# Kernel optimization log

Hardware: AMD Instinct MI355X
Metric: run time of the kernel (lower is better)

The kernel has to match this reference:

```python
import jax, jax.numpy as jnp
import numpy as np

BS, IN_SIZE, OUT_SIZE, FEATS = 32, 1024, 1024, 2048


def setup_inputs() -> dict:
    key = jax.random.key(0)
    kx, kw = jax.random.split(key)
    x = jax.random.normal(kx, (BS, IN_SIZE, FEATS), dtype=jnp.float32)
    # Per-sample weight matrices (the stacked nn.Parameters, kernel-size-1 conv
    # weights of shape [out_size, in_size, 1] -> squeezed to [out_size, in_size]).
    weights = jax.random.normal(kw, (BS, OUT_SIZE, IN_SIZE), dtype=jnp.float32)
    return {"x": x, "weights": weights}


def reference(x, weights):
    # F.conv2d(x.view(1, bs*in_size, feats), W.view(bs*out_size, in_size, 1), groups=bs)
    # with kernel size 1 is exactly a per-sample matmul:
    # out[b, o, f] = sum_i weights[b, o, i] * x[b, i, f]
    return jnp.einsum('boi,bif->bof', weights, x)
```

## Files before the change

### kernel.cpp

```cpp
#include <hip/hip_runtime.h>
#include <hip/hip_bf16.h>
#include <string.h>


typedef float  f32x2 __attribute__((ext_vector_type(2)));
typedef float  f32x4 __attribute__((ext_vector_type(4)));
typedef short  bf16x8 __attribute__((ext_vector_type(8)));
typedef unsigned int u32;

#define BATCH 32
#define MDIM 1024
#define KDIM 1024
#define NDIM 2048
#define BM 256
#define BN 256
#define BK 64
#define NT (KDIM / BK)
#define LSTR 68

__device__ __forceinline__ u32 cvt2(float a, float b) {
    float2 t; t.x = a; t.y = b;
    __hip_bfloat162 h = __float22bfloat162_rn(t);
    u32 r; memcpy(&r, &h, 4);
    return r;
}

__device__ __forceinline__ void lds_barrier() {
    asm volatile("s_waitcnt lgkmcnt(0)" ::: "memory");
    __builtin_amdgcn_s_barrier();
    asm volatile("" ::: "memory");
}

__global__ __launch_bounds__(512, 2) void bgemm_bf16_kernel(
    const float* __restrict__ x, const float* __restrict__ w,
    float* __restrict__ out)
{
    __shared__ unsigned short Ab[2][BM * LSTR];
    __shared__ unsigned short Bb[2][BN * LSTR];

    const int bid  = blockIdx.x;
    const int lbid = (bid & 7) * 128 + (bid >> 3);
    const int bx = lbid & 7;
    const int by = (lbid >> 3) & 3;
    const int bz = lbid >> 5;

    const int tid = threadIdx.x;
    const int m0  = by * BM;
    const int n0  = bx * BN;

    const int lane = tid & 63;
    const int wid  = tid >> 6;
    const int wm   = (wid >> 2) * 128;
    const int wn   = (wid & 3)  * 64;
    const int l15  = lane & 15;
    const int kg8  = (lane >> 4) * 8;

    const float* Ag = w + (size_t)bz * MDIM * KDIM + (size_t)m0 * KDIM;
    const float* Bg = x + (size_t)bz * KDIM * NDIM + n0;
    float*       Cg = out + (size_t)bz * MDIM * NDIM + (size_t)m0 * NDIM + n0;

    const int a_k4 = tid & 15;
    const int a_m0 = tid >> 4;
    int a_idx[8];
    #pragma unroll
    for (int i = 0; i < 8; ++i)
        a_idx[i] = (a_m0 + 32 * i) * LSTR + 4 * a_k4;
    const int bn0  = 2 * (tid & 127);
    const int b_k0 = 8 * (tid >> 7);
    int b_idx[2];
    #pragma unroll
    for (int c = 0; c < 2; ++c)
        b_idx[c] = (bn0 + c) * LSTR + b_k0;
    int rd_a[8], rd_b[4];
    #pragma unroll
    for (int mi = 0; mi < 8; ++mi)
        rd_a[mi] = (wm + mi * 16 + l15) * LSTR + kg8;
    #pragma unroll
    for (int ni = 0; ni < 4; ++ni)
        rd_b[ni] = (wn + ni * 16 + l15) * LSTR + kg8;

    const float* Ap = Ag + (size_t)a_m0 * KDIM + 4 * a_k4;
    const float* Bp = Bg + (size_t)b_k0 * NDIM + bn0;

    f32x4 acc[8][4];
    #pragma unroll
    for (int i = 0; i < 8; ++i)
        #pragma unroll
        for (int j = 0; j < 4; ++j)
            acc[i][j] = f32x4{0.f, 0.f, 0.f, 0.f};

    f32x4 aav[4];
    f32x2 bbv[8];

    auto load_regs = [&](int kt, int h) {
        #pragma unroll
        for (int i = 0; i < 4; ++i)
            aav[i] = *reinterpret_cast<const f32x4*>(
                Ap + (size_t)(32 * (i + 4 * h)) * KDIM + kt);
        #pragma unroll
        for (int j = 0; j < 8; ++j)
            bbv[j] = *reinterpret_cast<const f32x2*>(
                Bp + (size_t)(kt + 32 * h + j) * NDIM);
    };
    auto stage = [&](int s, int h) {
        #pragma unroll
        for (int i = 0; i < 4; ++i) {
            uint2 v = make_uint2(cvt2(aav[i][0], aav[i][1]),
                                 cvt2(aav[i][2], aav[i][3]));
            *reinterpret_cast<uint2*>(&Ab[s][a_idx[i + 4 * h]]) = v;
        }
        #pragma unroll
        for (int c = 0; c < 2; ++c) {
            uint4 v = make_uint4(cvt2(bbv[0][c], bbv[1][c]),
                                 cvt2(bbv[2][c], bbv[3][c]),
                                 cvt2(bbv[4][c], bbv[5][c]),
                                 cvt2(bbv[6][c], bbv[7][c]));
            *reinterpret_cast<uint4*>(&Bb[s][b_idx[c] + 32 * h]) = v;
        }
    };

    load_regs(0, 0);
    stage(0, 0);
    load_regs(0, 1);
    stage(0, 1);
    load_regs(BK, 0);
    lds_barrier();

    for (int t = 0; t < NT - 1; ++t) {
        const int cur = t & 1;
        const int ktn = (t + 1) * BK;
        bf16x8 bfr[4], af[4];

        #pragma unroll
        for (int ni = 0; ni < 4; ++ni)
            bfr[ni] = *reinterpret_cast<const bf16x8*>(&Bb[cur][rd_b[ni]]);
        #pragma unroll
        for (int mi = 0; mi < 4; ++mi)
            af[mi] = *reinterpret_cast<const bf16x8*>(&Ab[cur][rd_a[mi]]);

        stage(cur ^ 1, 0);
        load_regs(ktn, 1);

        __builtin_amdgcn_s_setprio(1);
        #pragma unroll
        for (int mi = 0; mi < 4; ++mi)
            #pragma unroll
            for (int ni = 0; ni < 4; ++ni)
                acc[mi][ni] = __builtin_amdgcn_mfma_f32_16x16x32_bf16(
                    af[mi], bfr[ni], acc[mi][ni], 0, 0, 0);
        __builtin_amdgcn_s_setprio(0);

        #pragma unroll
        for (int mi = 0; mi < 4; ++mi)
            af[mi] = *reinterpret_cast<const bf16x8*>(&Ab[cur][rd_a[mi + 4]]);

        __builtin_amdgcn_s_setprio(1);
        #pragma unroll
        for (int mi = 0; mi < 4; ++mi)
            #pragma unroll
            for (int ni = 0; ni < 4; ++ni)
                acc[mi + 4][ni] = __builtin_amdgcn_mfma_f32_16x16x32_bf16(
                    af[mi], bfr[ni], acc[mi + 4][ni], 0, 0, 0);
        __builtin_amdgcn_s_setprio(0);

        #pragma unroll
        for (int ni = 0; ni < 4; ++ni)
            bfr[ni] = *reinterpret_cast<const bf16x8*>(&Bb[cur][rd_b[ni] + 32]);
        #pragma unroll
        for (int mi = 0; mi < 4; ++mi)
            af[mi] = *reinterpret_cast<const bf16x8*>(&Ab[cur][rd_a[mi] + 32]);

        stage(cur ^ 1, 1);
        int kt2 = (t + 2) * BK;
        if (kt2 > KDIM - BK) kt2 = KDIM - BK;
        load_regs(kt2, 0);

        __builtin_amdgcn_s_setprio(1);
        #pragma unroll
        for (int mi = 0; mi < 4; ++mi)
            #pragma unroll
            for (int ni = 0; ni < 4; ++ni)
                acc[mi][ni] = __builtin_amdgcn_mfma_f32_16x16x32_bf16(
                    af[mi], bfr[ni], acc[mi][ni], 0, 0, 0);
        __builtin_amdgcn_s_setprio(0);

        #pragma unroll
        for (int mi = 0; mi < 4; ++mi)
            af[mi] = *reinterpret_cast<const bf16x8*>(&Ab[cur][rd_a[mi + 4] + 32]);

        __builtin_amdgcn_s_setprio(1);
        #pragma unroll
        for (int mi = 0; mi < 4; ++mi)
            #pragma unroll
            for (int ni = 0; ni < 4; ++ni)
                acc[mi + 4][ni] = __builtin_amdgcn_mfma_f32_16x16x32_bf16(
                    af[mi], bfr[ni], acc[mi + 4][ni], 0, 0, 0);
        __builtin_amdgcn_s_setprio(0);

        lds_barrier();
    }

    {
        const int cur = (NT - 1) & 1;
        #pragma unroll
        for (int kk = 0; kk < 2; ++kk) {
            bf16x8 bfr[4];
            #pragma unroll
            for (int ni = 0; ni < 4; ++ni)
                bfr[ni] = *reinterpret_cast<const bf16x8*>(
                    &Bb[cur][rd_b[ni] + 32 * kk]);
            #pragma unroll
            for (int mi = 0; mi < 8; ++mi) {
                bf16x8 af = *reinterpret_cast<const bf16x8*>(
                    &Ab[cur][rd_a[mi] + 32 * kk]);
                #pragma unroll
                for (int ni = 0; ni < 4; ++ni)
                    acc[mi][ni] = __builtin_amdgcn_mfma_f32_16x16x32_bf16(
                        af, bfr[ni], acc[mi][ni], 0, 0, 0);
            }
        }
    }

    const int rbase = (lane >> 4) * 4;
    #pragma unroll
    for (int mi = 0; mi < 8; ++mi) {
        #pragma unroll
        for (int ni = 0; ni < 4; ++ni) {
            int n  = wn + ni * 16 + l15;
            int mb = wm + mi * 16 + rbase;
            #pragma unroll
            for (int r = 0; r < 4; ++r)
                Cg[(size_t)(mb + r) * NDIM + n] = acc[mi][ni][r];
        }
    }
}

extern "C" void kernel_launch(void* const* d_in, const int* in_sizes, int n_in,
                              void* d_out, int out_size, void* d_ws, size_t ws_size,
                              hipStream_t stream) {
    const float* x = (const float*)d_in[0];
    const float* w = (const float*)d_in[1];
    float* out = (float*)d_out;
    const int nblocks = (NDIM / BN) * (MDIM / BM) * BATCH;
    bgemm_bf16_kernel<<<dim3(nblocks), dim3(512), 0, stream>>>(x, w, out);
}
```

Measured before the change: 231.9 us.

## Restructure main loop into barrier-separated load/stage/MFMA phases with split A/B loads

Splits the global-load and LDS-staging helpers into separate A and B versions and reorganizes each K iteration into four phases. Each phase issues LDS reads plus one global load or staging step, then an MFMA burst, with barriers around every burst. The goal is to keep waves in lock-step so memory and matrix work interleave across the waves of the workgroup, ping-pong style. In exchange it adds many more workgroup barriers per iteration and larger staging register arrays (8 A vectors, 16 B vectors), which may reduce occupancy or stall the MFMA pipe.

```diff
diff --git a/kernel.cpp b/kernel.cpp
--- a/kernel.cpp
+++ b/kernel.cpp
@@ -89,114 +89,106 @@
         for (int j = 0; j < 4; ++j)
             acc[i][j] = f32x4{0.f, 0.f, 0.f, 0.f};
 
-    f32x4 aav[4];
-    f32x2 bbv[8];
-
-    auto load_regs = [&](int kt, int h) {
-        #pragma unroll
-        for (int i = 0; i < 4; ++i)
+    f32x4 aav[8];
+    f32x2 bbv[16];
+
+    auto load_A = [&](int kt) {
+        #pragma unroll
+        for (int i = 0; i < 8; ++i)
             aav[i] = *reinterpret_cast<const f32x4*>(
-                Ap + (size_t)(32 * (i + 4 * h)) * KDIM + kt);
-        #pragma unroll
-        for (int j = 0; j < 8; ++j)
-            bbv[j] = *reinterpret_cast<const f32x2*>(
-                Bp + (size_t)(kt + 32 * h + j) * NDIM);
-    };
-    auto stage = [&](int s, int h) {
-        #pragma unroll
-        for (int i = 0; i < 4; ++i) {
+                Ap + (size_t)(32 * i) * KDIM + kt);
+    };
+    auto load_B = [&](int kt) {
+        #pragma unroll
+        for (int j = 0; j < 8; ++j) {
+            bbv[j]     = *reinterpret_cast<const f32x2*>(
+                Bp + (size_t)(kt + j) * NDIM);
+            bbv[j + 8] = *reinterpret_cast<const f32x2*>(
+                Bp + (size_t)(kt + 32 + j) * NDIM);
+        }
+    };
+    auto stage_A = [&](int s) {
+        #pragma unroll
+        for (int i = 0; i < 8; ++i) {
             uint2 v = make_uint2(cvt2(aav[i][0], aav[i][1]),
                                  cvt2(aav[i][2], aav[i][3]));
-            *reinterpret_cast<uint2*>(&Ab[s][a_idx[i + 4 * h]]) = v;
-        }
+            *reinterpret_cast<uint2*>(&Ab[s][a_idx[i]]) = v;
+        }
+    };
+    auto stage_B = [&](int s) {
         #pragma unroll
         for (int c = 0; c < 2; ++c) {
-            uint4 v = make_uint4(cvt2(bbv[0][c], bbv[1][c]),
-                                 cvt2(bbv[2][c], bbv[3][c]),
-                                 cvt2(bbv[4][c], bbv[5][c]),
-                                 cvt2(bbv[6][c], bbv[7][c]));
-            *reinterpret_cast<uint4*>(&Bb[s][b_idx[c] + 32 * h]) = v;
-        }
-    };
-
-    load_regs(0, 0);
-    stage(0, 0);
-    load_regs(0, 1);
-    stage(0, 1);
-    load_regs(BK, 0);
+            uint4 v0 = make_uint4(cvt2(bbv[0][c], bbv[1][c]),
+                                  cvt2(bbv[2][c], bbv[3][c]),
+                                  cvt2(bbv[4][c], bbv[5][c]),
+                                  cvt2(bbv[6][c], bbv[7][c]));
+            *reinterpret_cast<uint4*>(&Bb[s][b_idx[c]]) = v0;
+            uint4 v1 = make_uint4(cvt2(bbv[8][c],  bbv[9][c]),
+                                  cvt2(bbv[10][c], bbv[11][c]),
+                                  cvt2(bbv[12][c], bbv[13][c]),
+                                  cvt2(bbv[14][c], bbv[15][c]));
+            *reinterpret_cast<uint4*>(&Bb[s][b_idx[c] + 32]) = v1;
+        }
+    };
+    auto mfma4 = [&](int mb, const bf16x8* afr, const bf16x8* bfr) {
+        __builtin_amdgcn_s_setprio(1);
+        #pragma unroll
+        for (int mi = 0; mi < 4; ++mi)
+            #pragma unroll
+            for (int ni = 0; ni < 4; ++ni)
+                acc[mb + mi][ni] = __builtin_amdgcn_mfma_f32_16x16x32_bf16(
+                    afr[mi], bfr[ni], acc[mb + mi][ni], 0, 0, 0);
+        __builtin_amdgcn_s_setprio(0);
+    };
+
+    load_A(0);
+    load_B(0);
+    stage_A(0);
+    stage_B(0);
     lds_barrier();
 
     for (int t = 0; t < NT - 1; ++t) {
         const int cur = t & 1;
+        const int nxt = cur ^ 1;
         const int ktn = (t + 1) * BK;
-        bf16x8 bfr[4], af[4];
+        bf16x8 afr[4], bfr[4];
 
         #pragma unroll
         for (int ni = 0; ni < 4; ++ni)
             bfr[ni] = *reinterpret_cast<const bf16x8*>(&Bb[cur][rd_b[ni]]);
         #pragma unroll
         for (int mi = 0; mi < 4; ++mi)
-            af[mi] = *reinterpret_cast<const bf16x8*>(&Ab[cur][rd_a[mi]]);
-
-        stage(cur ^ 1, 0);
-        load_regs(ktn, 1);
-
-        __builtin_amdgcn_s_setprio(1);
-        #pragma unroll
-        for (int mi = 0; mi < 4; ++mi)
-            #pragma unroll
-            for (int ni = 0; ni < 4; ++ni)
-                acc[mi][ni] = __builtin_amdgcn_mfma_f32_16x16x32_bf16(
-                    af[mi], bfr[ni], acc[mi][ni], 0, 0, 0);
-        __builtin_amdgcn_s_setprio(0);
-
-        #pragma unroll
-        for (int mi = 0; mi < 4; ++mi)
-            af[mi] = *reinterpret_cast<const bf16x8*>(&Ab[cur][rd_a[mi + 4]]);
-
-        __builtin_amdgcn_s_setprio(1);
-        #pragma unroll
-        for (int mi = 0; mi < 4; ++mi)
-            #pragma unroll
-            for (int ni = 0; ni < 4; ++ni)
-                acc[mi + 4][ni] = __builtin_amdgcn_mfma_f32_16x16x32_bf16(
-                    af[mi], bfr[ni], acc[mi + 4][ni], 0, 0, 0);
-        __builtin_amdgcn_s_setprio(0);
+            afr[mi] = *reinterpret_cast<const bf16x8*>(&Ab[cur][rd_a[mi]]);
+        load_A(ktn);
+        lds_barrier();
+        mfma4(0, afr, bfr);
+        lds_barrier();
+
+        #pragma unroll
+        for (int mi = 0; mi < 4; ++mi)
+            afr[mi] = *reinterpret_cast<const bf16x8*>(&Ab[cur][rd_a[mi + 4]]);
+        stage_A(nxt);
+        load_B(ktn);
+        lds_barrier();
+        mfma4(4, afr, bfr);
+        lds_barrier();
 
         #pragma unroll
         for (int ni = 0; ni < 4; ++ni)
             bfr[ni] = *reinterpret_cast<const bf16x8*>(&Bb[cur][rd_b[ni] + 32]);
         #pragma unroll
         for (int mi = 0; mi < 4; ++mi)
-            af[mi] = *reinterpret_cast<const bf16x8*>(&Ab[cur][rd_a[mi] + 32]);
-
-        stage(cur ^ 1, 1);
-        int kt2 = (t + 2) * BK;
-        if (kt2 > KDIM - BK) kt2 = KDIM - BK;
-        load_regs(kt2, 0);
-
-        __builtin_amdgcn_s_setprio(1);
-        #pragma unroll
-        for (int mi = 0; mi < 4; ++mi)
-            #pragma unroll
-            for (int ni = 0; ni < 4; ++ni)
-                acc[mi][ni] = __builtin_amdgcn_mfma_f32_16x16x32_bf16(
-                    af[mi], bfr[ni], acc[mi][ni], 0, 0, 0);
-        __builtin_amdgcn_s_setprio(0);
-
-        #pragma unroll
-        for (int mi = 0; mi < 4; ++mi)
-            af[mi] = *reinterpret_cast<const bf16x8*>(&Ab[cur][rd_a[mi + 4] + 32]);
-
-        __builtin_amdgcn_s_setprio(1);
-        #pragma unroll
-        for (int mi = 0; mi < 4; ++mi)
-            #pragma unroll
-            for (int ni = 0; ni < 4; ++ni)
-                acc[mi + 4][ni] = __builtin_amdgcn_mfma_f32_16x16x32_bf16(
-                    af[mi], bfr[ni], acc[mi + 4][ni], 0, 0, 0);
-        __builtin_amdgcn_s_setprio(0);
-
+            afr[mi] = *reinterpret_cast<const bf16x8*>(&Ab[cur][rd_a[mi] + 32]);
+        stage_B(nxt);
+        lds_barrier();
+        mfma4(0, afr, bfr);
+        lds_barrier();
+
+        #pragma unroll
+        for (int mi = 0; mi < 4; ++mi)
+            afr[mi] = *reinterpret_cast<const bf16x8*>(&Ab[cur][rd_a[mi + 4] + 32]);
+        lds_barrier();
+        mfma4(4, afr, bfr);
         lds_barrier();
     }
 
```

New measurement: 323.1 us. +39.3%, slower.

## Pre-convert inputs to bf16 and stream tiles via direct global-to-LDS loads

Applied to the files above, without the earlier changes.

Adds two pre-pass kernels: one converts the weights to bf16, the other converts x to bf16 and transposes it to K-contiguous layout in the workspace. The GEMM then loads tiles with global_load_lds straight into swizzled LDS, which removes per-tile register staging and the in-loop conversion. The main loop is reorganised into four phases, each issuing a partial prefetch, with vmcnt waits and extra barriers between them. The cost is an extra fp32 read plus bf16 write of both inputs each call and more barriers. If the workspace is too small, an fp32 fallback kernel runs instead.

```diff
diff --git a/kernel.cpp b/kernel.cpp
--- a/kernel.cpp
+++ b/kernel.cpp
@@ -7,16 +7,12 @@
 typedef float  f32x4 __attribute__((ext_vector_type(4)));
 typedef short  bf16x8 __attribute__((ext_vector_type(8)));
 typedef unsigned int u32;
+typedef unsigned short u16;
 
 #define BATCH 32
 #define MDIM 1024
 #define KDIM 1024
 #define NDIM 2048
-#define BM 256
-#define BN 256
-#define BK 64
-#define NT (KDIM / BK)
-#define LSTR 68
 
 __device__ __forceinline__ u32 cvt2(float a, float b) {
     float2 t; t.x = a; t.y = b;
@@ -25,18 +21,68 @@
     return r;
 }
 
-__device__ __forceinline__ void lds_barrier() {
-    asm volatile("s_waitcnt lgkmcnt(0)" ::: "memory");
-    __builtin_amdgcn_s_barrier();
-    asm volatile("" ::: "memory");
-}
-
-__global__ __launch_bounds__(512, 2) void bgemm_bf16_kernel(
-    const float* __restrict__ x, const float* __restrict__ w,
+__global__ __launch_bounds__(256) void conv_w_kernel(
+    const float* __restrict__ w, u16* __restrict__ wb)
+{
+    const int nt = gridDim.x * blockDim.x;
+    const int total = BATCH * MDIM * KDIM / 4;
+    for (int i = blockIdx.x * blockDim.x + threadIdx.x; i < total; i += nt) {
+        f32x4 v = *reinterpret_cast<const f32x4*>(w + (size_t)i * 4);
+        uint2 p = make_uint2(cvt2(v[0], v[1]), cvt2(v[2], v[3]));
+        *reinterpret_cast<uint2*>(wb + (size_t)i * 4) = p;
+    }
+}
+
+__global__ __launch_bounds__(256) void conv_xt_kernel(
+    const float* __restrict__ x, u16* __restrict__ xb)
+{
+    __shared__ u16 tl[64][72];
+
+    const int bz = blockIdx.z;
+    const int k0 = blockIdx.y * 64;
+    const int n0 = blockIdx.x * 64;
+    const int t  = threadIdx.x;
+    const int a  = t >> 4;
+    const int b  = t & 15;
+
+    f32x4 v[4];
+    #pragma unroll
+    for (int i = 0; i < 4; ++i)
+        v[i] = *reinterpret_cast<const f32x4*>(
+            x + ((size_t)(bz * KDIM + k0 + 4 * a + i)) * NDIM + n0 + 4 * b);
+
+    #pragma unroll
+    for (int j = 0; j < 4; ++j) {
+        uint2 p = make_uint2(cvt2(v[0][j], v[1][j]), cvt2(v[2][j], v[3][j]));
+        *reinterpret_cast<uint2*>(&tl[4 * b + j][4 * a]) = p;
+    }
+    __syncthreads();
+
+    const int rn = t >> 2;
+    const int q  = t & 3;
+    u16* dst = xb + ((size_t)(bz * NDIM + n0 + rn)) * KDIM + k0 + 16 * q;
+    *reinterpret_cast<uint4*>(dst)     = *reinterpret_cast<uint4*>(&tl[rn][16 * q]);
+    *reinterpret_cast<uint4*>(dst + 8) = *reinterpret_cast<uint4*>(&tl[rn][16 * q + 8]);
+}
+
+#define BM 256
+#define BN 256
+#define BK 64
+#define NT2 (KDIM / BK)
+
+typedef __attribute__((address_space(1))) const unsigned char glob_u8;
+typedef __attribute__((address_space(3))) unsigned char lds_u8;
+
+__device__ __forceinline__ void gload16(const void* g, void* l) {
+    __builtin_amdgcn_global_load_lds((glob_u8*)g, (lds_u8*)l, 16, 0, 0);
+}
+
+__global__ __launch_bounds__(512, 2) void bgemm_4ph_kernel(
+    const u16* __restrict__ xb, const u16* __restrict__ wb,
     float* __restrict__ out)
 {
-    __shared__ unsigned short Ab[2][BM * LSTR];
-    __shared__ unsigned short Bb[2][BN * LSTR];
+    __shared__ u16 Al[2][16384];
+    __shared__ u16 Bl[2][16384];
 
     const int bid  = blockIdx.x;
     const int lbid = (bid & 7) * 128 + (bid >> 3);
@@ -44,43 +90,46 @@
     const int by = (lbid >> 3) & 3;
     const int bz = lbid >> 5;
 
-    const int tid = threadIdx.x;
-    const int m0  = by * BM;
-    const int n0  = bx * BN;
-
+    const int tid  = threadIdx.x;
+    const int wid  = tid >> 6;
     const int lane = tid & 63;
-    const int wid  = tid >> 6;
     const int wm   = (wid >> 2) * 128;
     const int wn   = (wid & 3)  * 64;
     const int l15  = lane & 15;
-    const int kg8  = (lane >> 4) * 8;
-
-    const float* Ag = w + (size_t)bz * MDIM * KDIM + (size_t)m0 * KDIM;
-    const float* Bg = x + (size_t)bz * KDIM * NDIM + n0;
-    float*       Cg = out + (size_t)bz * MDIM * NDIM + (size_t)m0 * NDIM + n0;
-
-    const int a_k4 = tid & 15;
-    const int a_m0 = tid >> 4;
-    int a_idx[8];
-    #pragma unroll
-    for (int i = 0; i < 8; ++i)
-        a_idx[i] = (a_m0 + 32 * i) * LSTR + 4 * a_k4;
-    const int bn0  = 2 * (tid & 127);
-    const int b_k0 = 8 * (tid >> 7);
-    int b_idx[2];
-    #pragma unroll
-    for (int c = 0; c < 2; ++c)
-        b_idx[c] = (bn0 + c) * LSTR + b_k0;
-    int rd_a[8], rd_b[4];
-    #pragma unroll
-    for (int mi = 0; mi < 8; ++mi)
-        rd_a[mi] = (wm + mi * 16 + l15) * LSTR + kg8;
-    #pragma unroll
-    for (int ni = 0; ni < 4; ++ni)
-        rd_b[ni] = (wn + ni * 16 + l15) * LSTR + kg8;
-
-    const float* Ap = Ag + (size_t)a_m0 * KDIM + 4 * a_k4;
-    const float* Bp = Bg + (size_t)b_k0 * NDIM + bn0;
+    const int h    = lane >> 4;
+
+    const int m0 = by * BM;
+    const int n0 = bx * BN;
+
+    const u16* Wb = wb + ((size_t)bz << 20);
+    const u16* Xb = xb + ((size_t)bz << 21);
+
+    const int srow = wid * 32 + (lane >> 2);
+    const int ssw  = 8 * ((lane & 3) ^ ((lane >> 2) & 3));
+    const u16* aSrc[2];
+    const u16* bSrc[2];
+    #pragma unroll
+    for (int i = 0; i < 2; ++i) {
+        aSrc[i] = Wb + (size_t)(m0 + srow + i * 16) * KDIM + ssw;
+        bSrc[i] = Xb + (size_t)(n0 + srow + i * 16) * KDIM + ssw;
+    }
+    const int ldst0 = wid * 1024 + 0 * 512;
+    const int ldst1 = wid * 1024 + 1 * 512;
+
+    int rdA[2][8], rdB[2][4];
+    #pragma unroll
+    for (int kk = 0; kk < 2; ++kk) {
+        #pragma unroll
+        for (int mi = 0; mi < 8; ++mi) {
+            int m = wm + mi * 16 + l15;
+            rdA[kk][mi] = kk * 8192 + m * 32 + 8 * (h ^ (m & 3));
+        }
+        #pragma unroll
+        for (int ni = 0; ni < 4; ++ni) {
+            int n = wn + ni * 16 + l15;
+            rdB[kk][ni] = kk * 8192 + n * 32 + 8 * (h ^ (n & 3));
+        }
+    }
 
     f32x4 acc[8][4];
     #pragma unroll
@@ -89,138 +138,102 @@
         for (int j = 0; j < 4; ++j)
             acc[i][j] = f32x4{0.f, 0.f, 0.f, 0.f};
 
-    f32x4 aav[4];
-    f32x2 bbv[8];
-
-    auto load_regs = [&](int kt, int h) {
-        #pragma unroll
-        for (int i = 0; i < 4; ++i)
-            aav[i] = *reinterpret_cast<const f32x4*>(
-                Ap + (size_t)(32 * (i + 4 * h)) * KDIM + kt);
-        #pragma unroll
-        for (int j = 0; j < 8; ++j)
-            bbv[j] = *reinterpret_cast<const f32x2*>(
-                Bp + (size_t)(kt + 32 * h + j) * NDIM);
-    };
-    auto stage = [&](int s, int h) {
-        #pragma unroll
-        for (int i = 0; i < 4; ++i) {
-            uint2 v = make_uint2(cvt2(aav[i][0], aav[i][1]),
-                                 cvt2(aav[i][2], aav[i][3]));
-            *reinterpret_cast<uint2*>(&Ab[s][a_idx[i + 4 * h]]) = v;
-        }
-        #pragma unroll
-        for (int c = 0; c < 2; ++c) {
-            uint4 v = make_uint4(cvt2(bbv[0][c], bbv[1][c]),
-                                 cvt2(bbv[2][c], bbv[3][c]),
-                                 cvt2(bbv[4][c], bbv[5][c]),
-                                 cvt2(bbv[6][c], bbv[7][c]));
-            *reinterpret_cast<uint4*>(&Bb[s][b_idx[c] + 32 * h]) = v;
-        }
-    };
-
-    load_regs(0, 0);
-    stage(0, 0);
-    load_regs(0, 1);
-    stage(0, 1);
-    load_regs(BK, 0);
-    lds_barrier();
-
-    for (int t = 0; t < NT - 1; ++t) {
-        const int cur = t & 1;
+    auto stageA = [&](int sb, int q, int kt) {
+        gload16(aSrc[0] + kt + q * 32, &Al[sb][q * 8192 + ldst0]);
+        gload16(aSrc[1] + kt + q * 32, &Al[sb][q * 8192 + ldst1]);
+    };
+    auto stageB = [&](int sb, int q, int kt) {
+        gload16(bSrc[0] + kt + q * 32, &Bl[sb][q * 8192 + ldst0]);
+        gload16(bSrc[1] + kt + q * 32, &Bl[sb][q * 8192 + ldst1]);
+    };
+
+    stageA(0, 0, 0);
+    stageB(0, 0, 0);
+    stageA(0, 1, 0);
+    stageB(0, 1, 0);
+    asm volatile("s_waitcnt vmcnt(4)" ::: "memory");
+    __builtin_amdgcn_s_barrier();
+
+    for (int t = 0; t < NT2; ++t) {
+        const int s   = t & 1;
+        const int sx  = s ^ 1;
         const int ktn = (t + 1) * BK;
-        bf16x8 bfr[4], af[4];
+        const bool st = (t + 1 < NT2);
+        bf16x8 afr[4], bfr[4];
 
         #pragma unroll
         for (int ni = 0; ni < 4; ++ni)
-            bfr[ni] = *reinterpret_cast<const bf16x8*>(&Bb[cur][rd_b[ni]]);
-        #pragma unroll
-        for (int mi = 0; mi < 4; ++mi)
-            af[mi] = *reinterpret_cast<const bf16x8*>(&Ab[cur][rd_a[mi]]);
-
-        stage(cur ^ 1, 0);
-        load_regs(ktn, 1);
-
+            bfr[ni] = *reinterpret_cast<const bf16x8*>(&Bl[s][rdB[0][ni]]);
+        #pragma unroll
+        for (int mi = 0; mi < 4; ++mi)
+            afr[mi] = *reinterpret_cast<const bf16x8*>(&Al[s][rdA[0][mi]]);
+        if (st) stageA(sx, 0, ktn);
+        __builtin_amdgcn_s_barrier();
         __builtin_amdgcn_s_setprio(1);
         #pragma unroll
         for (int mi = 0; mi < 4; ++mi)
             #pragma unroll
             for (int ni = 0; ni < 4; ++ni)
                 acc[mi][ni] = __builtin_amdgcn_mfma_f32_16x16x32_bf16(
-                    af[mi], bfr[ni], acc[mi][ni], 0, 0, 0);
+                    afr[mi], bfr[ni], acc[mi][ni], 0, 0, 0);
         __builtin_amdgcn_s_setprio(0);
-
-        #pragma unroll
-        for (int mi = 0; mi < 4; ++mi)
-            af[mi] = *reinterpret_cast<const bf16x8*>(&Ab[cur][rd_a[mi + 4]]);
-
+        __builtin_amdgcn_s_barrier();
+
+        #pragma unroll
+        for (int mi = 0; mi < 4; ++mi)
+            afr[mi] = *reinterpret_cast<const bf16x8*>(&Al[s][rdA[0][mi + 4]]);
+        if (st) stageB(sx, 0, ktn);
+        if (t == NT2 - 1)
+            asm volatile("s_waitcnt vmcnt(0)" ::: "memory");
+        else
+            asm volatile("s_waitcnt vmcnt(4)" ::: "memory");
+        __builtin_amdgcn_s_barrier();
         __builtin_amdgcn_s_setprio(1);
         #pragma unroll
         for (int mi = 0; mi < 4; ++mi)
             #pragma unroll
             for (int ni = 0; ni < 4; ++ni)
                 acc[mi + 4][ni] = __builtin_amdgcn_mfma_f32_16x16x32_bf16(
-                    af[mi], bfr[ni], acc[mi + 4][ni], 0, 0, 0);
+                    afr[mi], bfr[ni], acc[mi + 4][ni], 0, 0, 0);
         __builtin_amdgcn_s_setprio(0);
+        __builtin_amdgcn_s_barrier();
 
         #pragma unroll
         for (int ni = 0; ni < 4; ++ni)
-            bfr[ni] = *reinterpret_cast<const bf16x8*>(&Bb[cur][rd_b[ni] + 32]);
-        #pragma unroll
-        for (int mi = 0; mi < 4; ++mi)
-            af[mi] = *reinterpret_cast<const bf16x8*>(&Ab[cur][rd_a[mi] + 32]);
-
-        stage(cur ^ 1, 1);
-        int kt2 = (t + 2) * BK;
-        if (kt2 > KDIM - BK) kt2 = KDIM - BK;
-        load_regs(kt2, 0);
-
+            bfr[ni] = *reinterpret_cast<const bf16x8*>(&Bl[s][rdB[1][ni]]);
+        #pragma unroll
+        for (int mi = 0; mi < 4; ++mi)
+            afr[mi] = *reinterpret_cast<const bf16x8*>(&Al[s][rdA[1][mi]]);
+        if (st) stageA(sx, 1, ktn);
+        __builtin_amdgcn_s_barrier();
         __builtin_amdgcn_s_setprio(1);
         #pragma unroll
         for (int mi = 0; mi < 4; ++mi)
             #pragma unroll
             for (int ni = 0; ni < 4; ++ni)
                 acc[mi][ni] = __builtin_amdgcn_mfma_f32_16x16x32_bf16(
-                    af[mi], bfr[ni], acc[mi][ni], 0, 0, 0);
+                    afr[mi], bfr[ni], acc[mi][ni], 0, 0, 0);
         __builtin_amdgcn_s_setprio(0);
-
-        #pragma unroll
-        for (int mi = 0; mi < 4; ++mi)
-            af[mi] = *reinterpret_cast<const bf16x8*>(&Ab[cur][rd_a[mi + 4] + 32]);
-
+        __builtin_amdgcn_s_barrier();
+
+        #pragma unroll
+        for (int mi = 0; mi < 4; ++mi)
+            afr[mi] = *reinterpret_cast<const bf16x8*>(&Al[s][rdA[1][mi + 4]]);
+        if (st) stageB(sx, 1, ktn);
+        asm volatile("s_waitcnt vmcnt(4)" ::: "memory");
+        __builtin_amdgcn_s_barrier();
         __builtin_amdgcn_s_setprio(1);
         #pragma unroll
         for (int mi = 0; mi < 4; ++mi)
             #pragma unroll
             for (int ni = 0; ni < 4; ++ni)
                 acc[mi + 4][ni] = __builtin_amdgcn_mfma_f32_16x16x32_bf16(
-                    af[mi], bfr[ni], acc[mi + 4][ni], 0, 0, 0);
+                    afr[mi], bfr[ni], acc[mi + 4][ni], 0, 0, 0);
         __builtin_amdgcn_s_setprio(0);
-
-        lds_barrier();
-    }
-
-    {
-        const int cur = (NT - 1) & 1;
-        #pragma unroll
-        for (int kk = 0; kk < 2; ++kk) {
-            bf16x8 bfr[4];
-            #pragma unroll
-            for (int ni = 0; ni < 4; ++ni)
-                bfr[ni] = *reinterpret_cast<const bf16x8*>(
-                    &Bb[cur][rd_b[ni] + 32 * kk]);
-            #pragma unroll
-            for (int mi = 0; mi < 8; ++mi) {
-                bf16x8 af = *reinterpret_cast<const bf16x8*>(
-                    &Ab[cur][rd_a[mi] + 32 * kk]);
-                #pragma unroll
-                for (int ni = 0; ni < 4; ++ni)
-                    acc[mi][ni] = __builtin_amdgcn_mfma_f32_16x16x32_bf16(
-                        af, bfr[ni], acc[mi][ni], 0, 0, 0);
-            }
-        }
-    }
-
+        __builtin_amdgcn_s_barrier();
+    }
+
+    float* Cg = out + (size_t)bz * MDIM * NDIM + (size_t)(m0)*NDIM + n0;
     const int rbase = (lane >> 4) * 4;
     #pragma unroll
     for (int mi = 0; mi < 8; ++mi) {
@@ -233,6 +246,123 @@
                 Cg[(size_t)(mb + r) * NDIM + n] = acc[mi][ni][r];
         }
     }
+}
+
+#define FLSTR 68
+
+__device__ __forceinline__ void lds_barrier() {
+    asm volatile("s_waitcnt lgkmcnt(0)" ::: "memory");
+    __builtin_amdgcn_s_barrier();
+    asm volatile("" ::: "memory");
+}
+
+__global__ __launch_bounds__(512, 2) void bgemm_fb_kernel(
+    const float* __restrict__ x, const float* __restrict__ w,
+    float* __restrict__ out)
+{
+    __shared__ u16 Ab[2][BM * FLSTR];
+    __shared__ u16 Bb[2][BN * FLSTR];
+
+    const int bid  = blockIdx.x;
+    const int lbid = (bid & 7) * 128 + (bid >> 3);
+    const int bx = lbid & 7, by = (lbid >> 3) & 3, bz = lbid >> 5;
+    const int tid = threadIdx.x, lane = tid & 63, wid = tid >> 6;
+    const int wm = (wid >> 2) * 128, wn = (wid & 3) * 64;
+    const int l15 = lane & 15, kg8 = (lane >> 4) * 8;
+
+    const float* Ag = w + (size_t)bz * MDIM * KDIM + (size_t)(by * BM) * KDIM;
+    const float* Bg = x + (size_t)bz * KDIM * NDIM + bx * BN;
+    float* Cg = out + (size_t)bz * MDIM * NDIM + (size_t)(by * BM) * NDIM + bx * BN;
+
+    const int a_k4 = tid & 15, a_m0 = tid >> 4;
+    int a_idx[8];
+    #pragma unroll
+    for (int i = 0; i < 8; ++i) a_idx[i] = (a_m0 + 32 * i) * FLSTR + 4 * a_k4;
+    const int bn0 = 2 * (tid & 127), b_k0 = 8 * (tid >> 7);
+    int b_idx[2];
+    #pragma unroll
+    for (int c = 0; c < 2; ++c) b_idx[c] = (bn0 + c) * FLSTR + b_k0;
+    int rd_a[8], rd_b[4];
+    #pragma unroll
+    for (int mi = 0; mi < 8; ++mi) rd_a[mi] = (wm + mi * 16 + l15) * FLSTR + kg8;
+    #pragma unroll
+    for (int ni = 0; ni < 4; ++ni) rd_b[ni] = (wn + ni * 16 + l15) * FLSTR + kg8;
+
+    const float* Ap = Ag + (size_t)a_m0 * KDIM + 4 * a_k4;
+    const float* Bp = Bg + (size_t)b_k0 * NDIM + bn0;
+
+    f32x4 acc[8][4];
+    #pragma unroll
+    for (int i = 0; i < 8; ++i)
+        #pragma unroll
+        for (int j = 0; j < 4; ++j) acc[i][j] = f32x4{0.f, 0.f, 0.f, 0.f};
+
+    f32x4 aav[4]; f32x2 bbv[8];
+    auto load_regs = [&](int kt, int hh) {
+        #pragma unroll
+        for (int i = 0; i < 4; ++i)
+            aav[i] = *reinterpret_cast<const f32x4*>(Ap + (size_t)(32 * (i + 4 * hh)) * KDIM + kt);
+        #pragma unroll
+        for (int j = 0; j < 8; ++j)
+            bbv[j] = *reinterpret_cast<const f32x2*>(Bp + (size_t)(kt + 32 * hh + j) * NDIM);
+    };
+    auto stage = [&](int s, int hh) {
+        #pragma unroll
+        for (int i = 0; i < 4; ++i) {
+            uint2 v = make_uint2(cvt2(aav[i][0], aav[i][1]), cvt2(aav[i][2], aav[i][3]));
+            *reinterpret_cast<uint2*>(&Ab[s][a_idx[i + 4 * hh]]) = v;
+        }
+        #pragma unroll
+        for (int c = 0; c < 2; ++c) {
+            uint4 v = make_uint4(cvt2(bbv[0][c], bbv[1][c]), cvt2(bbv[2][c], bbv[3][c]),
+                                 cvt2(bbv[4][c], bbv[5][c]), cvt2(bbv[6][c], bbv[7][c]));
+            *reinterpret_cast<uint4*>(&Bb[s][b_idx[c] + 32 * hh]) = v;
+        }
+    };
+    auto mfma_half = [&](int s, int kk, int mb) {
+        bf16x8 bfr[4], af[4];
+        #pragma unroll
+        for (int ni = 0; ni < 4; ++ni)
+            bfr[ni] = *reinterpret_cast<const bf16x8*>(&Bb[s][rd_b[ni] + 32 * kk]);
+        #pragma unroll
+        for (int mi = 0; mi < 4; ++mi)
+            af[mi] = *reinterpret_cast<const bf16x8*>(&Ab[s][rd_a[mi + mb] + 32 * kk]);
+        #pragma unroll
+        for (int mi = 0; mi < 4; ++mi)
+            #pragma unroll
+            for (int ni = 0; ni < 4; ++ni)
+                acc[mi + mb][ni] = __builtin_amdgcn_mfma_f32_16x16x32_bf16(
+                    af[mi], bfr[ni], acc[mi + mb][ni], 0, 0, 0);
+    };
+
+    load_regs(0, 0); stage(0, 0); load_regs(0, 1); stage(0, 1); load_regs(BK, 0);
+    lds_barrier();
+    for (int t = 0; t < NT2 - 1; ++t) {
+        const int cur = t & 1;
+        stage(cur ^ 1, 0);
+        load_regs((t + 1) * BK, 1);
+        mfma_half(cur, 0, 0); mfma_half(cur, 0, 4);
+        stage(cur ^ 1, 1);
+        int kt2 = (t + 2) * BK; if (kt2 > KDIM - BK) kt2 = KDIM - BK;
+        load_regs(kt2, 0);
+        mfma_half(cur, 1, 0); mfma_half(cur, 1, 4);
+        lds_barrier();
+    }
+    {
+        const int cur = (NT2 - 1) & 1;
+        mfma_half(cur, 0, 0); mfma_half(cur, 0, 4);
+        mfma_half(cur, 1, 0); mfma_half(cur, 1, 4);
+    }
+    const int rbase = (lane >> 4) * 4;
+    #pragma unroll
+    for (int mi = 0; mi < 8; ++mi)
+        #pragma unroll
+        for (int ni = 0; ni < 4; ++ni) {
+            int n = wn + ni * 16 + l15, mb = wm + mi * 16 + rbase;
+            #pragma unroll
+            for (int r = 0; r < 4; ++r)
+                Cg[(size_t)(mb + r) * NDIM + n] = acc[mi][ni][r];
+        }
 }
 
 extern "C" void kernel_launch(void* const* d_in, const int* in_sizes, int n_in,
@@ -241,6 +371,16 @@
     const float* x = (const float*)d_in[0];
     const float* w = (const float*)d_in[1];
     float* out = (float*)d_out;
-    const int nblocks = (NDIM / BN) * (MDIM / BM) * BATCH;
-    bgemm_bf16_kernel<<<dim3(nblocks), dim3(512), 0, stream>>>(x, w, out);
-}
+
+    const size_t need = (size_t)BATCH * MDIM * KDIM * 2
+                      + (size_t)BATCH * NDIM * KDIM * 2;
+    if (ws_size >= need) {
+        u16* wb = (u16*)d_ws;
+        u16* xb = wb + (size_t)BATCH * MDIM * KDIM;
+        conv_w_kernel<<<dim3(2048), dim3(256), 0, stream>>>(w, wb);
+        conv_xt_kernel<<<dim3(NDIM / 64, KDIM / 64, BATCH), dim3(256), 0, stream>>>(x, xb);
+        bgemm_4ph_kernel<<<dim3((NDIM / BN) * (MDIM / BM) * BATCH), dim3(512), 0, stream>>>(xb, wb, out);
+    } else {
+        bgemm_fb_kernel<<<dim3((NDIM / BN) * (MDIM / BM) * BATCH), dim3(512), 0, stream>>>(x, w, out);
+    }
+}
```

Result: slower. 346.1 us (+49.2%).
